# Performance work log

Hardware: AMD Instinct MI355X
Metric: run time of the kernel (lower is better)

## Reference

```python
import jax, jax.numpy as jnp
import numpy as np

RES = 192      # resolution
RANK = 8       # low-rank
FD = 32        # feature_dim
NFPD = 32      # num_features_per_dim = round(32768**(1/3))
RADIUS = 1.3
NI = 128       # n_intersections
STEP = 0.0352  # step_size
B = 2048       # rays


def setup_inputs():
    key = jax.random.key(0)
    ks = jax.random.split(key, 12)
    ro = jax.random.normal(ks[0], (B, 3), dtype=jnp.float32)
    ro = ro / jnp.linalg.norm(ro, axis=-1, keepdims=True) * 2.5  # origins outside the cube
    rd = -ro + 0.1 * jax.random.normal(ks[1], (B, 3), dtype=jnp.float32)
    rd = rd / jnp.linalg.norm(rd, axis=-1, keepdims=True)        # roughly toward origin
    def nrm(k, shape, std):
        return std * jax.random.normal(k, shape, dtype=jnp.float32)
    return {
        "rays_o": ro, "rays_d": rd,
        "Gxy": nrm(ks[2], (RES, RES, 3, RANK), 0.1),
        "Gxz": nrm(ks[3], (RES, RES, 3, RANK), 0.1),
        "Gyz": nrm(ks[4], (RES, RES, 3, RANK), 0.1),
        "F_grid": nrm(ks[5], (NFPD, NFPD, NFPD, FD), 0.05),
        "sW0": nrm(ks[6], (FD, 128), FD ** -0.5),
        "sW1": nrm(ks[7], (128, 128), 128 ** -0.5),
        "sW2": nrm(ks[8], (128, 16), 128 ** -0.5),
        "cW0": nrm(ks[9], (31, 64), 31 ** -0.5),
        "cW1": nrm(ks[10], (64, 64), 64 ** -0.5),
        "cW2": nrm(ks[11], (64, 3), 64 ** -0.5),
    }


def trilinear(vol, coords):
    # vol: [D,H,W,C]; coords: [N,3] as (x,y,z) in [-1,1]; x indexes W (last spatial dim)
    # matches torch grid_sample(align_corners=True, mode='bilinear', padding_mode='border')
    D, H, W, C = vol.shape
    def prep(c, size):
        idx = jnp.clip((c + 1.0) * 0.5 * (size - 1), 0.0, size - 1.0)  # border clamp
        i0 = jnp.clip(jnp.floor(idx).astype(jnp.int32), 0, size - 2)
        return i0, i0 + 1, idx - i0
    x0, x1, wx = prep(coords[:, 0], W)
    y0, y1, wy = prep(coords[:, 1], H)
    z0, z1, wz = prep(coords[:, 2], D)
    wx = wx[:, None]; wy = wy[:, None]; wz = wz[:, None]
    def g(zi, yi, xi):
        return vol[zi, yi, xi]  # [N,C]
    c00 = g(z0, y0, x0) * (1 - wx) + g(z0, y0, x1) * wx
    c01 = g(z0, y1, x0) * (1 - wx) + g(z0, y1, x1) * wx
    c10 = g(z1, y0, x0) * (1 - wx) + g(z1, y0, x1) * wx
    c11 = g(z1, y1, x0) * (1 - wx) + g(z1, y1, x1) * wx
    c0 = c00 * (1 - wy) + c01 * wy
    c1 = c10 * (1 - wy) + c11 * wy
    return c0 * (1 - wz) + c1 * wz


def sh16(d):
    # tcnn SphericalHarmonics degree 4 on directions (input (d+1)/2 is unmapped back to d internally)
    x, y, z = d[:, 0], d[:, 1], d[:, 2]
    x2, y2, z2 = x * x, y * y, z * z
    return jnp.stack([
        jnp.full_like(x, 0.28209479177387814),
        -0.48860251190291987 * y,
        0.48860251190291987 * z,
        -0.48860251190291987 * x,
        1.0925484305920792 * x * y,
        -1.0925484305920792 * y * z,
        0.94617469575755997 * z2 - 0.31539156525251999,
        -1.0925484305920792 * x * z,
        0.54627421529603959 * (x2 - y2),
        0.59004358992664352 * y * (-3.0 * x2 + y2),
        2.8906114426405538 * x * y * z,
        0.45704579946446572 * y * (1.0 - 5.0 * z2),
        0.3731763325901154 * z * (5.0 * z2 - 3.0),
        0.45704579946446572 * x * (1.0 - 5.0 * z2),
        1.445305721320277 * z * (x2 - y2),
        0.59004358992664352 * x * (-x2 + 3.0 * y2),
    ], axis=-1)


def _forward(rays_o, rays_d, Gxy, Gxz, Gyz, F_grid, sW0, sW1, sW2, cW0, cW1, cW2):
    b = rays_o.shape[0]
    # --- get_intersections: ray/AABB [-R,R]^3, uniform marching ---
    d = jnp.where(jnp.abs(rays_d) < 1e-9, 1e-9, rays_d)
    t1 = (-RADIUS - rays_o) / d
    t2 = (RADIUS - rays_o) / d
    tmin = jnp.max(jnp.minimum(t1, t2), axis=-1)
    tmax = jnp.min(jnp.maximum(t1, t2), axis=-1)
    near = jnp.maximum(tmin, 0.0)
    ts = near[:, None] + jnp.arange(NI + 1, dtype=jnp.float32) * STEP  # intersections [B,NI+1]
    tmid = 0.5 * (ts[:, :-1] + ts[:, 1:])                              # [B,NI]
    pts = rays_o[:, None, :] + tmid[..., None] * rays_d[:, None, :]    # [B,NI,3]
    mask = (jnp.all(jnp.abs(pts) <= RADIUS, axis=-1)
            & (tmid <= tmax[:, None]) & (tmax > tmin)[:, None])        # [B,NI]
    rdn = rays_d / jnp.linalg.norm(rays_d, axis=-1, keepdims=True)
    # coordinate chain of forward + eval_pts nets out to pts/RADIUS in [-1,1]
    p = ((pts / RADIUS + 1.0) * RES / 2.0) * 2.0 / RES - 1.0
    pf = p.reshape(-1, 3)
    # --- densify low-rank tri-plane grid: sum_r Gxy*Gxz*Gyz -> [RES,RES,RES,3] ---
    grid = jnp.zeros((RES, RES, RES, 3), dtype=Gxy.dtype)
    for r in range(RANK):  # fixed small rank; avoids a [RES^3,3,RANK] intermediate
        grid = grid + (Gxy[:, :, None, :, r] * Gxz[:, None, :, :, r] * Gyz[None, :, :, :, r])
    # --- eval_pts: grid_sample -> hash-feature grid_sample -> MLPs ---
    Gvals = trilinear(grid, pf)            # [N,3]
    Fvals = trilinear(F_grid, Gvals)       # [N,FD]
    h = jax.nn.relu(Fvals @ sW0)
    h = jax.nn.relu(h @ sW1)
    out16 = h @ sW2                        # [N,16]
    sigma = out16[:, 0].reshape(b, NI)
    sigma = jax.nn.relu(jnp.where(mask, sigma, 0.0))
    rdn_pts = jnp.broadcast_to(rdn[:, None, :], (b, NI, 3)).reshape(-1, 3)
    ci = jnp.concatenate([sh16(rdn_pts), out16[:, 1:]], axis=-1)  # [N,31]
    c = jax.nn.relu(ci @ cW0)
    c = jax.nn.relu(c @ cW1)
    color = (c @ cW2).reshape(b, NI, 3)
    color = jnp.where(mask[..., None], color, 0.0)
    # --- sigma2alpha + shrgb2rgb (white background) ---
    dists = ts[:, 1:] - ts[:, :-1]         # |rdn| == 1
    alpha = 1.0 - jnp.exp(-sigma * dists)
    T = jnp.cumprod(1.0 - alpha + 1e-10, axis=-1)
    T = jnp.concatenate([jnp.ones_like(T[:, :1]), T[:, :-1]], axis=-1)  # exclusive
    w = alpha * T                          # abs_light [B,NI]
    rgb = jax.nn.sigmoid(color)
    acc = jnp.sum(w, axis=-1)
    return jnp.sum(w[..., None] * rgb, axis=1) + (1.0 - acc)[..., None]  # [B,3]


def reference(rays_o, rays_d, Gxy, Gxz, Gyz, F_grid, sW0, sW1, sW2, cW0, cW1, cW2):
    return _forward(rays_o, rays_d, Gxy, Gxz, Gyz, F_grid, sW0, sW1, sW2, cW0, cW1, cW2)
```

## Files before the change

kernel.cpp:

```cpp
#include <hip/hip_runtime.h>
#include <math.h>

#define RES 192
#define RANK 8
#define NI 128
#define LW 136

typedef __attribute__((ext_vector_type(8))) _Float16 h8;
typedef __attribute__((ext_vector_type(2))) _Float16 h2f;
typedef __attribute__((ext_vector_type(4))) float floatx4;

#define OFF_SW0 0
#define OFF_SW1 4096
#define OFF_SW2 20480
#define OFF_CW0 22528
#define OFF_CW1 24576
#define OFF_CW2 28672
#define PACK_TOTAL 29696

#define TRI_CELLS (RES*RES)
#define TRI_TOTAL (3*TRI_CELLS*24)
#define FG_TOTAL  (32*32*32*32)
#define PREP_TOTAL (PACK_TOTAL + TRI_TOTAL + FG_TOTAL)

__device__ __forceinline__ void prep_idx(float c, int size, int& i0, float& f){
    float idx = (c + 1.0f)*0.5f*(float)(size-1);
    idx = fminf(fmaxf(idx, 0.0f), (float)(size-1));
    int ii = (int)idx;
    if (ii > size-2) ii = size-2;
    i0 = ii;
    f = idx - (float)ii;
}

__device__ __forceinline__ float wred64(float v){
    #pragma unroll
    for (int o=32;o>0;o>>=1) v += __shfl_down(v, o, 64);
    return v;
}

__global__ void __launch_bounds__(256) prep_all(
    const float* __restrict__ sW0, const float* __restrict__ sW1,
    const float* __restrict__ sW2, const float* __restrict__ cW0,
    const float* __restrict__ cW1, const float* __restrict__ cW2,
    const float* __restrict__ Gxy, const float* __restrict__ Gxz,
    const float* __restrict__ Gyz, const float* __restrict__ F_grid,
    _Float16* __restrict__ Wp, _Float16* __restrict__ Gp, _Float16* __restrict__ Fg)
{
    int e = blockIdx.x*256 + threadIdx.x;
    if (e < PACK_TOTAL){
        const float* src; int K, N, ksteps, base;
        if      (e < OFF_SW1){ src=sW0; K=32;  N=128; ksteps=1; base=OFF_SW0; }
        else if (e < OFF_SW2){ src=sW1; K=128; N=128; ksteps=4; base=OFF_SW1; }
        else if (e < OFF_CW0){ src=sW2; K=128; N=16;  ksteps=4; base=OFF_SW2; }
        else if (e < OFF_CW1){ src=cW0; K=31;  N=64;  ksteps=1; base=OFF_CW0; }
        else if (e < OFF_CW2){ src=cW1; K=64;  N=64;  ksteps=2; base=OFF_CW1; }
        else                 { src=cW2; K=64;  N=3;   ksteps=2; base=OFF_CW2; }
        int i = e - base;
        int j = i & 7, lane = (i>>3)&63, t = i>>9;
        int ks = t % ksteps, nt = t / ksteps;
        int k = ks*32 + (lane>>4)*8 + j;
        int n = nt*16 + (lane&15);
        float v = (k < K && n < N) ? src[k*N + n] : 0.0f;
        Wp[e] = (_Float16)v;
        return;
    }
    int e2 = e - PACK_TOTAL;
    if (e2 < TRI_TOTAL){
        int p    = e2 / (TRI_CELLS*24);
        int rem  = e2 - p*(TRI_CELLS*24);
        int cell = rem / 24;
        int c    = rem - cell*24;
        const float* src = (p==0) ? Gxy : (p==1) ? Gxz : Gyz;
        Gp[((size_t)(p*TRI_CELLS + cell))*32 + c] = (_Float16)src[(size_t)cell*24 + c];
        return;
    }
    int e3 = e2 - TRI_TOTAL;
    Fg[e3] = (_Float16)F_grid[e3];
}

__launch_bounds__(256, 4)
__global__ void nerf_fused(
    const float* __restrict__ rays_o, const float* __restrict__ rays_d,
    const _Float16* __restrict__ Gp, const _Float16* __restrict__ Fg,
    const _Float16* __restrict__ Wp, float* __restrict__ out)
{
    __shared__ _Float16 buf[128*LW];
    __shared__ float sigmaArr[128];
    __shared__ float rgbArr[128*3];
    __shared__ float wtot[2];
    __shared__ float partial[8];

    const int tid  = threadIdx.x;
    const int lane = tid & 63;
    const int wv   = tid >> 6;
    const int ray  = blockIdx.x;

    const float ox = rays_o[ray*3+0], oy = rays_o[ray*3+1], oz = rays_o[ray*3+2];
    const float dx = rays_d[ray*3+0], dy = rays_d[ray*3+1], dz = rays_d[ray*3+2];

    float sdx = (fabsf(dx) < 1e-9f) ? 1e-9f : dx;
    float sdy = (fabsf(dy) < 1e-9f) ? 1e-9f : dy;
    float sdz = (fabsf(dz) < 1e-9f) ? 1e-9f : dz;
    float t1x = (-1.3f - ox)/sdx, t2x = (1.3f - ox)/sdx;
    float t1y = (-1.3f - oy)/sdy, t2y = (1.3f - oy)/sdy;
    float t1z = (-1.3f - oz)/sdz, t2z = (1.3f - oz)/sdz;
    float tmin = fmaxf(fminf(t1x,t2x), fmaxf(fminf(t1y,t2y), fminf(t1z,t2z)));
    float tmax = fminf(fmaxf(t1x,t2x), fminf(fmaxf(t1y,t2y), fmaxf(t1z,t2z)));
    float nearv = fmaxf(tmin, 0.0f);

    const int rowbase = wv*32;
    const int col  = lane & 15;
    const int quad = lane >> 4;
    const int ar0  = rowbase + col;
    const int ar1  = ar0 + 16;

    {
        int sid = rowbase + (lane & 31);
        float w_ts0 = nearv + (float)sid     * 0.0352f;
        float w_ts1 = nearv + (float)(sid+1) * 0.0352f;
        float w_tm  = 0.5f*(w_ts0+w_ts1);
        float wpx = ox + w_tm*dx, wpy = oy + w_tm*dy, wpz = oz + w_tm*dz;
        bool m = (fabsf(wpx)<=1.3f) && (fabsf(wpy)<=1.3f) && (fabsf(wpz)<=1.3f)
               && (w_tm<=tmax) && (tmax>tmin);
        if (__ballot(m) == 0ULL) goto composite;
    }

    {
        const int s = rowbase + (lane >> 1);
        const int h = lane & 1;

        float ts0 = nearv + (float)s     * 0.0352f;
        float ts1 = nearv + (float)(s+1) * 0.0352f;
        float tmid = 0.5f*(ts0+ts1);
        float px = ox + tmid*dx, py = oy + tmid*dy, pz = oz + tmid*dz;
        bool mask = (fabsf(px)<=1.3f) && (fabsf(py)<=1.3f) && (fabsf(pz)<=1.3f)
                  && (tmid<=tmax) && (tmax>tmin);

        h8 FVa = {0,0,0,0,0,0,0,0};
        h8 FVb = {0,0,0,0,0,0,0,0};

        if (mask){
            float p0 = (px/1.3f + 1.0f)*192.0f/2.0f*2.0f/192.0f - 1.0f;
            float p1 = (py/1.3f + 1.0f)*192.0f/2.0f*2.0f/192.0f - 1.0f;
            float p2 = (pz/1.3f + 1.0f)*192.0f/2.0f*2.0f/192.0f - 1.0f;

            int x0, y0, z0; float fx, fy, fz;
            prep_idx(p0, RES, x0, fx);
            prep_idx(p1, RES, y0, fy);
            prep_idx(p2, RES, z0, fz);

            const int zi = z0 + h;
            const float wzc = h ? fz : (1.0f - fz);

            h8 XY[2][3], XZ[2][3], YZ[2][2][3];
            {
                const h8* pxy0 = (const h8*)(Gp + ((size_t)(zi*RES + y0  ))*32);
                const h8* pxy1 = (const h8*)(Gp + ((size_t)(zi*RES + y0+1))*32);
                const h8* pxz0 = (const h8*)(Gp + ((size_t)(TRI_CELLS + zi*RES + x0  ))*32);
                const h8* pxz1 = (const h8*)(Gp + ((size_t)(TRI_CELLS + zi*RES + x0+1))*32);
                const h8* pyz00 = (const h8*)(Gp + ((size_t)(2*TRI_CELLS + (y0  )*RES + x0  ))*32);
                const h8* pyz01 = (const h8*)(Gp + ((size_t)(2*TRI_CELLS + (y0  )*RES + x0+1))*32);
                const h8* pyz10 = (const h8*)(Gp + ((size_t)(2*TRI_CELLS + (y0+1)*RES + x0  ))*32);
                const h8* pyz11 = (const h8*)(Gp + ((size_t)(2*TRI_CELLS + (y0+1)*RES + x0+1))*32);
                #pragma unroll
                for (int q=0;q<3;q++){
                    XY[0][q]=pxy0[q]; XY[1][q]=pxy1[q];
                    XZ[0][q]=pxz0[q]; XZ[1][q]=pxz1[q];
                    YZ[0][0][q]=pyz00[q]; YZ[0][1][q]=pyz01[q];
                    YZ[1][0][q]=pyz10[q]; YZ[1][1][q]=pyz11[q];
                }
            }

            h8 ACC0 = {0,0,0,0,0,0,0,0};
            h8 ACC1 = {0,0,0,0,0,0,0,0};
            h8 ACC2 = {0,0,0,0,0,0,0,0};
            #pragma unroll
            for (int yc=0; yc<2; yc++){
                const float wy = yc ? fy : (1.0f - fy);
                #pragma unroll
                for (int xc=0; xc<2; xc++){
                    const float wx = xc ? fx : (1.0f - fx);
                    const _Float16 wh = (_Float16)(wzc*wy*wx);
                    const h8 w8 = {wh,wh,wh,wh,wh,wh,wh,wh};
                    h8 Q0 = (XY[yc][0]*XZ[xc][0])*YZ[yc][xc][0];
                    h8 Q1 = (XY[yc][1]*XZ[xc][1])*YZ[yc][xc][1];
                    h8 Q2 = (XY[yc][2]*XZ[xc][2])*YZ[yc][xc][2];
                    ACC0 = __builtin_elementwise_fma(Q0, w8, ACC0);
                    ACC1 = __builtin_elementwise_fma(Q1, w8, ACC1);
                    ACC2 = __builtin_elementwise_fma(Q2, w8, ACC2);
                }
            }
            h2f a0h = __builtin_shufflevector(ACC0,ACC0,0,1) + __builtin_shufflevector(ACC0,ACC0,2,3);
            h2f b0h = __builtin_shufflevector(ACC0,ACC0,4,5) + __builtin_shufflevector(ACC0,ACC0,6,7);
            h2f c0h = a0h + b0h;
            float gv0 = (float)c0h[0] + (float)c0h[1];
            h2f a1h = __builtin_shufflevector(ACC1,ACC1,0,1) + __builtin_shufflevector(ACC1,ACC1,2,3);
            h2f b1h = __builtin_shufflevector(ACC1,ACC1,4,5) + __builtin_shufflevector(ACC1,ACC1,6,7);
            h2f c1h = a1h + b1h;
            float gv1 = (float)c1h[0] + (float)c1h[1];
            h2f a2h = __builtin_shufflevector(ACC2,ACC2,0,1) + __builtin_shufflevector(ACC2,ACC2,2,3);
            h2f b2h = __builtin_shufflevector(ACC2,ACC2,4,5) + __builtin_shufflevector(ACC2,ACC2,6,7);
            h2f c2h = a2h + b2h;
            float gv2 = (float)c2h[0] + (float)c2h[1];

            gv0 += __shfl_xor(gv0, 1, 64);
            gv1 += __shfl_xor(gv1, 1, 64);
            gv2 += __shfl_xor(gv2, 1, 64);

            int a0,b0,c0; float fa,fb,fc;
            prep_idx(gv2, 32, a0, fa);
            prep_idx(gv1, 32, b0, fb);
            prep_idx(gv0, 32, c0, fc);
            #pragma unroll
            for (int zc=0; zc<2; zc++){
                const int zi2 = a0+zc; const float wz2 = zc ? fa : 1.f-fa;
                #pragma unroll
                for (int yc=0; yc<2; yc++){
                    const int yi2 = b0+yc; const float wy2 = yc ? fb : 1.f-fb;
                    #pragma unroll
                    for (int xc=0; xc<2; xc++){
                        const int xi2 = c0+xc; const float wx2 = xc ? fc : 1.f-fc;
                        const _Float16 wh = (_Float16)(wz2*wy2*wx2);
                        const h8 w8 = {wh,wh,wh,wh,wh,wh,wh,wh};
                        const h8* pf = (const h8*)(Fg + ((size_t)((zi2*32+yi2)*32+xi2))*32 + h*16);
                        FVa = __builtin_elementwise_fma(pf[0], w8, FVa);
                        FVb = __builtin_elementwise_fma(pf[1], w8, FVb);
                    }
                }
            }
        }

        *(h8*)&buf[s*LW + h*16]     = FVa;
        *(h8*)&buf[s*LW + h*16 + 8] = FVb;
    }

    {
        h8 a0 = *(const h8*)&buf[ar0*LW + quad*8];
        h8 a1 = *(const h8*)&buf[ar1*LW + quad*8];
        const h8* W = (const h8*)(Wp + OFF_SW0);
        #pragma unroll
        for (int nt=0; nt<8; nt++){
            h8 b = W[nt*64 + lane];
            floatx4 c0v = {0.f,0.f,0.f,0.f}, c1v = {0.f,0.f,0.f,0.f};
            c0v = __builtin_amdgcn_mfma_f32_16x16x32_f16(a0, b, c0v, 0,0,0);
            c1v = __builtin_amdgcn_mfma_f32_16x16x32_f16(a1, b, c1v, 0,0,0);
            #pragma unroll
            for (int r=0;r<4;r++){
                int row0 = rowbase + quad*4 + r;
                buf[row0*LW      + nt*16 + col] = (_Float16)fmaxf(c0v[r],0.f);
                buf[(row0+16)*LW + nt*16 + col] = (_Float16)fmaxf(c1v[r],0.f);
            }
        }
    }

    {
        h8 A0[4], A1[4];
        #pragma unroll
        for (int ks=0;ks<4;ks++){
            A0[ks] = *(const h8*)&buf[ar0*LW + ks*32 + quad*8];
            A1[ks] = *(const h8*)&buf[ar1*LW + ks*32 + quad*8];
        }
        const h8* W = (const h8*)(Wp + OFF_SW1);
        #pragma unroll
        for (int nt=0; nt<8; nt++){
            floatx4 c0v = {0.f,0.f,0.f,0.f}, c1v = {0.f,0.f,0.f,0.f};
            #pragma unroll
            for (int ks=0;ks<4;ks++){
                h8 b = W[(nt*4+ks)*64 + lane];
                c0v = __builtin_amdgcn_mfma_f32_16x16x32_f16(A0[ks], b, c0v, 0,0,0);
                c1v = __builtin_amdgcn_mfma_f32_16x16x32_f16(A1[ks], b, c1v, 0,0,0);
            }
            #pragma unroll
            for (int r=0;r<4;r++){
                int row0 = rowbase + quad*4 + r;
                buf[row0*LW      + nt*16 + col] = (_Float16)fmaxf(c0v[r],0.f);
                buf[(row0+16)*LW + nt*16 + col] = (_Float16)fmaxf(c1v[r],0.f);
            }
        }
    }

    {
        h8 A0[4], A1[4];
        #pragma unroll
        for (int ks=0;ks<4;ks++){
            A0[ks] = *(const h8*)&buf[ar0*LW + ks*32 + quad*8];
            A1[ks] = *(const h8*)&buf[ar1*LW + ks*32 + quad*8];
        }
        const h8* W = (const h8*)(Wp + OFF_SW2);
        floatx4 c0v = {0.f,0.f,0.f,0.f}, c1v = {0.f,0.f,0.f,0.f};
        #pragma unroll
        for (int ks=0;ks<4;ks++){
            h8 b = W[ks*64 + lane];
            c0v = __builtin_amdgcn_mfma_f32_16x16x32_f16(A0[ks], b, c0v, 0,0,0);
            c1v = __builtin_amdgcn_mfma_f32_16x16x32_f16(A1[ks], b, c1v, 0,0,0);
        }
        #pragma unroll
        for (int r=0;r<4;r++){
            int row0 = rowbase + quad*4 + r;
            if (col == 0){
                sigmaArr[row0]    = c0v[r];
                sigmaArr[row0+16] = c1v[r];
            } else {
                buf[row0*LW      + 15 + col] = (_Float16)c0v[r];
                buf[(row0+16)*LW + 15 + col] = (_Float16)c1v[r];
            }
        }
        const float dn = sqrtf(dx*dx+dy*dy+dz*dz);
        const float X = dx/dn, Y = dy/dn, Z = dz/dn;
        const float X2=X*X, Y2=Y*Y, Z2=Z*Z;
        float sh[16];
        sh[0]= 0.28209479177387814f;
        sh[1]=-0.48860251190291987f*Y;
        sh[2]= 0.48860251190291987f*Z;
        sh[3]=-0.48860251190291987f*X;
        sh[4]= 1.0925484305920792f*X*Y;
        sh[5]=-1.0925484305920792f*Y*Z;
        sh[6]= 0.94617469575756f*Z2 - 0.31539156525252f;
        sh[7]=-1.0925484305920792f*X*Z;
        sh[8]= 0.5462742152960396f*(X2-Y2);
        sh[9]= 0.5900435899266435f*Y*(-3.0f*X2+Y2);
        sh[10]=2.890611442640554f*X*Y*Z;
        sh[11]=0.4570457994644657f*Y*(1.0f-5.0f*Z2);
        sh[12]=0.3731763325901154f*Z*(5.0f*Z2-3.0f);
        sh[13]=0.4570457994644657f*X*(1.0f-5.0f*Z2);
        sh[14]=1.445305721320277f*Z*(X2-Y2);
        sh[15]=0.5900435899266435f*X*(-X2+3.0f*Y2);
        if (lane < 32){
            int row = rowbase + lane;
            #pragma unroll
            for (int k=0;k<16;k++) buf[row*LW + k] = (_Float16)sh[k];
        }
    }

    {
        h8 a0 = *(const h8*)&buf[ar0*LW + quad*8];
        h8 a1 = *(const h8*)&buf[ar1*LW + quad*8];
        const h8* W = (const h8*)(Wp + OFF_CW0);
        #pragma unroll
        for (int nt=0; nt<4; nt++){
            h8 b = W[nt*64 + lane];
            floatx4 c0v = {0.f,0.f,0.f,0.f}, c1v = {0.f,0.f,0.f,0.f};
            c0v = __builtin_amdgcn_mfma_f32_16x16x32_f16(a0, b, c0v, 0,0,0);
            c1v = __builtin_amdgcn_mfma_f32_16x16x32_f16(a1, b, c1v, 0,0,0);
            #pragma unroll
            for (int r=0;r<4;r++){
                int row0 = rowbase + quad*4 + r;
                buf[row0*LW      + nt*16 + col] = (_Float16)fmaxf(c0v[r],0.f);
                buf[(row0+16)*LW + nt*16 + col] = (_Float16)fmaxf(c1v[r],0.f);
            }
        }
    }

    {
        h8 A0[2], A1[2];
        #pragma unroll
        for (int ks=0;ks<2;ks++){
            A0[ks] = *(const h8*)&buf[ar0*LW + ks*32 + quad*8];
            A1[ks] = *(const h8*)&buf[ar1*LW + ks*32 + quad*8];
        }
        const h8* W = (const h8*)(Wp + OFF_CW1);
        #pragma unroll
        for (int nt=0; nt<4; nt++){
            floatx4 c0v = {0.f,0.f,0.f,0.f}, c1v = {0.f,0.f,0.f,0.f};
            #pragma unroll
            for (int ks=0;ks<2;ks++){
                h8 b = W[(nt*2+ks)*64 + lane];
                c0v = __builtin_amdgcn_mfma_f32_16x16x32_f16(A0[ks], b, c0v, 0,0,0);
                c1v = __builtin_amdgcn_mfma_f32_16x16x32_f16(A1[ks], b, c1v, 0,0,0);
            }
            #pragma unroll
            for (int r=0;r<4;r++){
                int row0 = rowbase + quad*4 + r;
                buf[row0*LW      + nt*16 + col] = (_Float16)fmaxf(c0v[r],0.f);
                buf[(row0+16)*LW + nt*16 + col] = (_Float16)fmaxf(c1v[r],0.f);
            }
        }
    }

    {
        h8 A0[2], A1[2];
        #pragma unroll
        for (int ks=0;ks<2;ks++){
            A0[ks] = *(const h8*)&buf[ar0*LW + ks*32 + quad*8];
            A1[ks] = *(const h8*)&buf[ar1*LW + ks*32 + quad*8];
        }
        const h8* W = (const h8*)(Wp + OFF_CW2);
        floatx4 c0v = {0.f,0.f,0.f,0.f}, c1v = {0.f,0.f,0.f,0.f};
        #pragma unroll
        for (int ks=0;ks<2;ks++){
            h8 b = W[ks*64 + lane];
            c0v = __builtin_amdgcn_mfma_f32_16x16x32_f16(A0[ks], b, c0v, 0,0,0);
            c1v = __builtin_amdgcn_mfma_f32_16x16x32_f16(A1[ks], b, c1v, 0,0,0);
        }
        if (col < 3){
            #pragma unroll
            for (int r=0;r<4;r++){
                int row0 = rowbase + quad*4 + r;
                rgbArr[row0*3 + col]      = c0v[r];
                rgbArr[(row0+16)*3 + col] = c1v[r];
            }
        }
    }

composite:
    __syncthreads();

    {
        float alpha = 0.f, rr = 0.f, rg = 0.f, rb = 0.f;
        if (tid < 128){
            float ts0 = nearv + (float)tid     * 0.0352f;
            float ts1 = nearv + (float)(tid+1) * 0.0352f;
            float tmid = 0.5f*(ts0+ts1);
            float dist = ts1 - ts0;
            float px = ox + tmid*dx, py = oy + tmid*dy, pz = oz + tmid*dz;
            bool mask = (fabsf(px)<=1.3f) && (fabsf(py)<=1.3f) && (fabsf(pz)<=1.3f)
                      && (tmid<=tmax) && (tmax>tmin);
            float sg = mask ? fmaxf(sigmaArr[tid], 0.f) : 0.f;
            alpha = 1.0f - expf(-sg*dist);
            if (mask){
                rr = 1.0f/(1.0f+expf(-rgbArr[tid*3+0]));
                rg = 1.0f/(1.0f+expf(-rgbArr[tid*3+1]));
                rb = 1.0f/(1.0f+expf(-rgbArr[tid*3+2]));
            }
        }
        float p = 1.0f - alpha + 1e-10f;
        #pragma unroll
        for (int off=1; off<64; off<<=1){
            float u = __shfl_up(p, off, 64);
            if (lane >= off) p *= u;
        }
        if (tid < 128 && lane == 63) wtot[wv] = p;
        float excl = __shfl_up(p, 1, 64);
        if (lane == 0) excl = 1.0f;
        __syncthreads();
        if (tid < 128){
            float T = excl;
            if (wv == 1) T *= wtot[0];
            float w = alpha * T;
            float v0 = wred64(w*rr);
            float v1 = wred64(w*rg);
            float v2 = wred64(w*rb);
            float v3 = wred64(w);
            if (lane == 0){
                partial[wv*4+0]=v0; partial[wv*4+1]=v1; partial[wv*4+2]=v2; partial[wv*4+3]=v3;
            }
        }
        __syncthreads();
        if (tid == 0){
            float acc = partial[3] + partial[7];
            float bg  = 1.0f - acc;
            out[ray*3+0] = partial[0] + partial[4] + bg;
            out[ray*3+1] = partial[1] + partial[5] + bg;
            out[ray*3+2] = partial[2] + partial[6] + bg;
        }
    }
}

extern "C" void kernel_launch(void* const* d_in, const int* in_sizes, int n_in,
                              void* d_out, int out_size, void* d_ws, size_t ws_size,
                              hipStream_t stream){
    const float* rays_o = (const float*)d_in[0];
    const float* rays_d = (const float*)d_in[1];
    const float* Gxy    = (const float*)d_in[2];
    const float* Gxz    = (const float*)d_in[3];
    const float* Gyz    = (const float*)d_in[4];
    const float* F_grid = (const float*)d_in[5];
    const float* sW0    = (const float*)d_in[6];
    const float* sW1    = (const float*)d_in[7];
    const float* sW2    = (const float*)d_in[8];
    const float* cW0    = (const float*)d_in[9];
    const float* cW1    = (const float*)d_in[10];
    const float* cW2    = (const float*)d_in[11];

    _Float16* Wp = (_Float16*)d_ws;
    _Float16* Gp = Wp + PACK_TOTAL;
    _Float16* Fg = Gp + (size_t)3*TRI_CELLS*32;

    prep_all<<<PREP_TOTAL/256, 256, 0, stream>>>(sW0,sW1,sW2,cW0,cW1,cW2,
                                                 Gxy,Gxz,Gyz,F_grid, Wp,Gp,Fg);
    nerf_fused<<<2048, 256, 0, stream>>>(rays_o, rays_d, Gp, Fg, Wp, (float*)d_out);
}
```

Measured before the change: 131.5 us.

## Split each ray's samples across eight waves with four lanes per sample

Doubles the block to 512 threads so each wave handles 16 samples instead of 32. Four lanes now cooperate on each sample: they split the (z,y) corners of the tri-plane gather and combine results with xor shuffles, and each takes an 8-channel slice of the feature-grid trilinear gather. The MLP stages then issue one MFMA row-tile per wave instead of two. The aim is more wavefronts to hide gather latency and fewer registers per thread. The cost is more shuffle reductions, possibly lower occupancy per CU because of the larger block and LDS use, and idle upper waves during compositing.

Result: slower. 138.8 us (+5.6%).

```diff
diff --git a/kernel.cpp b/kernel.cpp
--- a/kernel.cpp
+++ b/kernel.cpp
@@ -36,6 +36,13 @@
     #pragma unroll
     for (int o=32;o>0;o>>=1) v += __shfl_down(v, o, 64);
     return v;
+}
+
+__device__ __forceinline__ float hsum8(h8 a){
+    h2f x = __builtin_shufflevector(a,a,0,1) + __builtin_shufflevector(a,a,2,3);
+    h2f y = __builtin_shufflevector(a,a,4,5) + __builtin_shufflevector(a,a,6,7);
+    h2f z = x + y;
+    return (float)z[0] + (float)z[1];
 }
 
 __global__ void __launch_bounds__(256) prep_all(
@@ -78,7 +85,7 @@
     Fg[e3] = (_Float16)F_grid[e3];
 }
 
-__launch_bounds__(256, 4)
+__launch_bounds__(512, 8)
 __global__ void nerf_fused(
     const float* __restrict__ rays_o, const float* __restrict__ rays_d,
     const _Float16* __restrict__ Gp, const _Float16* __restrict__ Fg,
@@ -95,6 +102,11 @@
     const int wv   = tid >> 6;
     const int ray  = blockIdx.x;
 
+    const int rowbase = wv*16;
+    const int col  = lane & 15;
+    const int quad = lane >> 4;
+    const int ar   = rowbase + col;
+
     const float ox = rays_o[ray*3+0], oy = rays_o[ray*3+1], oz = rays_o[ray*3+2];
     const float dx = rays_d[ray*3+0], dy = rays_d[ray*3+1], dz = rays_d[ray*3+2];
 
@@ -108,316 +120,248 @@
     float tmax = fminf(fmaxf(t1x,t2x), fminf(fmaxf(t1y,t2y), fmaxf(t1z,t2z)));
     float nearv = fmaxf(tmin, 0.0f);
 
-    const int rowbase = wv*32;
-    const int col  = lane & 15;
-    const int quad = lane >> 4;
-    const int ar0  = rowbase + col;
-    const int ar1  = ar0 + 16;
-
-    {
-        int sid = rowbase + (lane & 31);
-        float w_ts0 = nearv + (float)sid     * 0.0352f;
-        float w_ts1 = nearv + (float)(sid+1) * 0.0352f;
-        float w_tm  = 0.5f*(w_ts0+w_ts1);
-        float wpx = ox + w_tm*dx, wpy = oy + w_tm*dy, wpz = oz + w_tm*dz;
-        bool m = (fabsf(wpx)<=1.3f) && (fabsf(wpy)<=1.3f) && (fabsf(wpz)<=1.3f)
-               && (w_tm<=tmax) && (tmax>tmin);
-        if (__ballot(m) == 0ULL) goto composite;
+    const int s   = rowbase + (lane >> 2);
+    const int sub = lane & 3;
+    const int zc  = sub & 1;
+    const int yc  = sub >> 1;
+
+    float ts0 = nearv + (float)s     * 0.0352f;
+    float ts1 = nearv + (float)(s+1) * 0.0352f;
+    float tmid = 0.5f*(ts0+ts1);
+    float px = ox + tmid*dx, py = oy + tmid*dy, pz = oz + tmid*dz;
+    bool mask = (fabsf(px)<=1.3f) && (fabsf(py)<=1.3f) && (fabsf(pz)<=1.3f)
+              && (tmid<=tmax) && (tmax>tmin);
+
+    if (__ballot(mask) != 0ULL){
+        {
+            h8 FV = {0,0,0,0,0,0,0,0};
+            if (mask){
+                float p0 = (px/1.3f + 1.0f)*192.0f/2.0f*2.0f/192.0f - 1.0f;
+                float p1 = (py/1.3f + 1.0f)*192.0f/2.0f*2.0f/192.0f - 1.0f;
+                float p2 = (pz/1.3f + 1.0f)*192.0f/2.0f*2.0f/192.0f - 1.0f;
+
+                int x0, y0, z0; float fx, fy, fz;
+                prep_idx(p0, RES, x0, fx);
+                prep_idx(p1, RES, y0, fy);
+                prep_idx(p2, RES, z0, fz);
+
+                const int zi = z0 + zc;
+                const int yi = y0 + yc;
+                const float wzy = (zc ? fz : 1.0f-fz) * (yc ? fy : 1.0f-fy);
+
+                h8 XYc[3], XZ0[3], XZ1[3], YZ0[3], YZ1[3];
+                {
+                    const h8* pxy = (const h8*)(Gp + ((size_t)(zi*RES + yi))*32);
+                    const h8* px0 = (const h8*)(Gp + ((size_t)(TRI_CELLS + zi*RES + x0  ))*32);
+                    const h8* px1 = (const h8*)(Gp + ((size_t)(TRI_CELLS + zi*RES + x0+1))*32);
+                    const h8* py0 = (const h8*)(Gp + ((size_t)(2*TRI_CELLS + yi*RES + x0  ))*32);
+                    const h8* py1 = (const h8*)(Gp + ((size_t)(2*TRI_CELLS + yi*RES + x0+1))*32);
+                    #pragma unroll
+                    for (int q=0;q<3;q++){
+                        XYc[q]=pxy[q];
+                        XZ0[q]=px0[q]; XZ1[q]=px1[q];
+                        YZ0[q]=py0[q]; YZ1[q]=py1[q];
+                    }
+                }
+
+                h8 ACC0, ACC1, ACC2;
+                {
+                    const _Float16 w0 = (_Float16)(wzy*(1.0f-fx));
+                    const _Float16 w1 = (_Float16)(wzy*fx);
+                    const h8 w80 = {w0,w0,w0,w0,w0,w0,w0,w0};
+                    const h8 w81 = {w1,w1,w1,w1,w1,w1,w1,w1};
+                    ACC0 = (XYc[0]*XZ0[0])*YZ0[0]*w80;
+                    ACC1 = (XYc[1]*XZ0[1])*YZ0[1]*w80;
+                    ACC2 = (XYc[2]*XZ0[2])*YZ0[2]*w80;
+                    ACC0 = __builtin_elementwise_fma((XYc[0]*XZ1[0])*YZ1[0], w81, ACC0);
+                    ACC1 = __builtin_elementwise_fma((XYc[1]*XZ1[1])*YZ1[1], w81, ACC1);
+                    ACC2 = __builtin_elementwise_fma((XYc[2]*XZ1[2])*YZ1[2], w81, ACC2);
+                }
+                float gv0 = hsum8(ACC0);
+                float gv1 = hsum8(ACC1);
+                float gv2 = hsum8(ACC2);
+                gv0 += __shfl_xor(gv0, 1, 64); gv0 += __shfl_xor(gv0, 2, 64);
+                gv1 += __shfl_xor(gv1, 1, 64); gv1 += __shfl_xor(gv1, 2, 64);
+                gv2 += __shfl_xor(gv2, 1, 64); gv2 += __shfl_xor(gv2, 2, 64);
+
+                int a0,b0,c0; float fa,fb,fc;
+                prep_idx(gv2, 32, a0, fa);
+                prep_idx(gv1, 32, b0, fb);
+                prep_idx(gv0, 32, c0, fc);
+                #pragma unroll
+                for (int zc2=0; zc2<2; zc2++){
+                    const int zi2 = a0+zc2; const float wz2 = zc2 ? fa : 1.f-fa;
+                    #pragma unroll
+                    for (int yc2=0; yc2<2; yc2++){
+                        const int yi2 = b0+yc2; const float wy2 = yc2 ? fb : 1.f-fb;
+                        #pragma unroll
+                        for (int xc2=0; xc2<2; xc2++){
+                            const int xi2 = c0+xc2; const float wx2 = xc2 ? fc : 1.f-fc;
+                            const _Float16 wh = (_Float16)(wz2*wy2*wx2);
+                            const h8 w8 = {wh,wh,wh,wh,wh,wh,wh,wh};
+                            const h8* pf = (const h8*)(Fg + ((size_t)((zi2*32+yi2)*32+xi2))*32 + sub*8);
+                            FV = __builtin_elementwise_fma(pf[0], w8, FV);
+                        }
+                    }
+                }
+            }
+            *(h8*)&buf[s*LW + sub*8] = FV;
+        }
+
+        {
+            h8 a = *(const h8*)&buf[ar*LW + quad*8];
+            const h8* W = (const h8*)(Wp + OFF_SW0);
+            #pragma unroll
+            for (int nt=0; nt<8; nt++){
+                h8 b = W[nt*64 + lane];
+                floatx4 cv = {0.f,0.f,0.f,0.f};
+                cv = __builtin_amdgcn_mfma_f32_16x16x32_f16(a, b, cv, 0,0,0);
+                #pragma unroll
+                for (int r=0;r<4;r++){
+                    int row = rowbase + quad*4 + r;
+                    buf[row*LW + nt*16 + col] = (_Float16)fmaxf(cv[r],0.f);
+                }
+            }
+        }
+
+        {
+            h8 A[4];
+            #pragma unroll
+            for (int ks=0;ks<4;ks++) A[ks] = *(const h8*)&buf[ar*LW + ks*32 + quad*8];
+            const h8* W = (const h8*)(Wp + OFF_SW1);
+            #pragma unroll
+            for (int nt=0; nt<8; nt++){
+                floatx4 cv = {0.f,0.f,0.f,0.f};
+                #pragma unroll
+                for (int ks=0;ks<4;ks++){
+                    h8 b = W[(nt*4+ks)*64 + lane];
+                    cv = __builtin_amdgcn_mfma_f32_16x16x32_f16(A[ks], b, cv, 0,0,0);
+                }
+                #pragma unroll
+                for (int r=0;r<4;r++){
+                    int row = rowbase + quad*4 + r;
+                    buf[row*LW + nt*16 + col] = (_Float16)fmaxf(cv[r],0.f);
+                }
+            }
+        }
+
+        {
+            h8 A[4];
+            #pragma unroll
+            for (int ks=0;ks<4;ks++) A[ks] = *(const h8*)&buf[ar*LW + ks*32 + quad*8];
+            const h8* W = (const h8*)(Wp + OFF_SW2);
+            floatx4 cv = {0.f,0.f,0.f,0.f};
+            #pragma unroll
+            for (int ks=0;ks<4;ks++){
+                h8 b = W[ks*64 + lane];
+                cv = __builtin_amdgcn_mfma_f32_16x16x32_f16(A[ks], b, cv, 0,0,0);
+            }
+            #pragma unroll
+            for (int r=0;r<4;r++){
+                int row = rowbase + quad*4 + r;
+                if (col == 0) sigmaArr[row] = cv[r];
+                else          buf[row*LW + 15 + col] = (_Float16)cv[r];
+            }
+            const float dn = sqrtf(dx*dx+dy*dy+dz*dz);
+            const float X = dx/dn, Y = dy/dn, Z = dz/dn;
+            const float X2=X*X, Y2=Y*Y, Z2=Z*Z;
+            float sh[16];
+            sh[0]= 0.28209479177387814f;
+            sh[1]=-0.48860251190291987f*Y;
+            sh[2]= 0.48860251190291987f*Z;
+            sh[3]=-0.48860251190291987f*X;
+            sh[4]= 1.0925484305920792f*X*Y;
+            sh[5]=-1.0925484305920792f*Y*Z;
+            sh[6]= 0.94617469575756f*Z2 - 0.31539156525252f;
+            sh[7]=-1.0925484305920792f*X*Z;
+            sh[8]= 0.5462742152960396f*(X2-Y2);
+            sh[9]= 0.5900435899266435f*Y*(-3.0f*X2+Y2);
+            sh[10]=2.890611442640554f*X*Y*Z;
+            sh[11]=0.4570457994644657f*Y*(1.0f-5.0f*Z2);
+            sh[12]=0.3731763325901154f*Z*(5.0f*Z2-3.0f);
+            sh[13]=0.4570457994644657f*X*(1.0f-5.0f*Z2);
+            sh[14]=1.445305721320277f*Z*(X2-Y2);
+            sh[15]=0.5900435899266435f*X*(-X2+3.0f*Y2);
+            if (lane < 16){
+                int row = rowbase + lane;
+                #pragma unroll
+                for (int k=0;k<16;k++) buf[row*LW + k] = (_Float16)sh[k];
+            }
+        }
+
+        {
+            h8 a = *(const h8*)&buf[ar*LW + quad*8];
+            const h8* W = (const h8*)(Wp + OFF_CW0);
+            #pragma unroll
+            for (int nt=0; nt<4; nt++){
+                h8 b = W[nt*64 + lane];
+                floatx4 cv = {0.f,0.f,0.f,0.f};
+                cv = __builtin_amdgcn_mfma_f32_16x16x32_f16(a, b, cv, 0,0,0);
+                #pragma unroll
+                for (int r=0;r<4;r++){
+                    int row = rowbase + quad*4 + r;
+                    buf[row*LW + nt*16 + col] = (_Float16)fmaxf(cv[r],0.f);
+                }
+            }
+        }
+
+        {
+            h8 A[2];
+            #pragma unroll
+            for (int ks=0;ks<2;ks++) A[ks] = *(const h8*)&buf[ar*LW + ks*32 + quad*8];
+            const h8* W = (const h8*)(Wp + OFF_CW1);
+            #pragma unroll
+            for (int nt=0; nt<4; nt++){
+                floatx4 cv = {0.f,0.f,0.f,0.f};
+                #pragma unroll
+                for (int ks=0;ks<2;ks++){
+                    h8 b = W[(nt*2+ks)*64 + lane];
+                    cv = __builtin_amdgcn_mfma_f32_16x16x32_f16(A[ks], b, cv, 0,0,0);
+                }
+                #pragma unroll
+                for (int r=0;r<4;r++){
+                    int row = rowbase + quad*4 + r;
+                    buf[row*LW + nt*16 + col] = (_Float16)fmaxf(cv[r],0.f);
+                }
+            }
+        }
+
+        {
+            h8 A[2];
+            #pragma unroll
+            for (int ks=0;ks<2;ks++) A[ks] = *(const h8*)&buf[ar*LW + ks*32 + quad*8];
+            const h8* W = (const h8*)(Wp + OFF_CW2);
+            floatx4 cv = {0.f,0.f,0.f,0.f};
+            #pragma unroll
+            for (int ks=0;ks<2;ks++){
+                h8 b = W[ks*64 + lane];
+                cv = __builtin_amdgcn_mfma_f32_16x16x32_f16(A[ks], b, cv, 0,0,0);
+            }
+            if (col < 3){
+                #pragma unroll
+                for (int r=0;r<4;r++){
+                    int row = rowbase + quad*4 + r;
+                    rgbArr[row*3 + col] = cv[r];
+                }
+            }
+        }
     }
 
-    {
-        const int s = rowbase + (lane >> 1);
-        const int h = lane & 1;
-
-        float ts0 = nearv + (float)s     * 0.0352f;
-        float ts1 = nearv + (float)(s+1) * 0.0352f;
-        float tmid = 0.5f*(ts0+ts1);
-        float px = ox + tmid*dx, py = oy + tmid*dy, pz = oz + tmid*dz;
-        bool mask = (fabsf(px)<=1.3f) && (fabsf(py)<=1.3f) && (fabsf(pz)<=1.3f)
-                  && (tmid<=tmax) && (tmax>tmin);
-
-        h8 FVa = {0,0,0,0,0,0,0,0};
-        h8 FVb = {0,0,0,0,0,0,0,0};
-
-        if (mask){
-            float p0 = (px/1.3f + 1.0f)*192.0f/2.0f*2.0f/192.0f - 1.0f;
-            float p1 = (py/1.3f + 1.0f)*192.0f/2.0f*2.0f/192.0f - 1.0f;
-            float p2 = (pz/1.3f + 1.0f)*192.0f/2.0f*2.0f/192.0f - 1.0f;
-
-            int x0, y0, z0; float fx, fy, fz;
-            prep_idx(p0, RES, x0, fx);
-            prep_idx(p1, RES, y0, fy);
-            prep_idx(p2, RES, z0, fz);
-
-            const int zi = z0 + h;
-            const float wzc = h ? fz : (1.0f - fz);
-
-            h8 XY[2][3], XZ[2][3], YZ[2][2][3];
-            {
-                const h8* pxy0 = (const h8*)(Gp + ((size_t)(zi*RES + y0  ))*32);
-                const h8* pxy1 = (const h8*)(Gp + ((size_t)(zi*RES + y0+1))*32);
-                const h8* pxz0 = (const h8*)(Gp + ((size_t)(TRI_CELLS + zi*RES + x0  ))*32);
-                const h8* pxz1 = (const h8*)(Gp + ((size_t)(TRI_CELLS + zi*RES + x0+1))*32);
-                const h8* pyz00 = (const h8*)(Gp + ((size_t)(2*TRI_CELLS + (y0  )*RES + x0  ))*32);
-                const h8* pyz01 = (const h8*)(Gp + ((size_t)(2*TRI_CELLS + (y0  )*RES + x0+1))*32);
-                const h8* pyz10 = (const h8*)(Gp + ((size_t)(2*TRI_CELLS + (y0+1)*RES + x0  ))*32);
-                const h8* pyz11 = (const h8*)(Gp + ((size_t)(2*TRI_CELLS + (y0+1)*RES + x0+1))*32);
-                #pragma unroll
-                for (int q=0;q<3;q++){
-                    XY[0][q]=pxy0[q]; XY[1][q]=pxy1[q];
-                    XZ[0][q]=pxz0[q]; XZ[1][q]=pxz1[q];
-                    YZ[0][0][q]=pyz00[q]; YZ[0][1][q]=pyz01[q];
-                    YZ[1][0][q]=pyz10[q]; YZ[1][1][q]=pyz11[q];
-                }
-            }
-
-            h8 ACC0 = {0,0,0,0,0,0,0,0};
-            h8 ACC1 = {0,0,0,0,0,0,0,0};
-            h8 ACC2 = {0,0,0,0,0,0,0,0};
-            #pragma unroll
-            for (int yc=0; yc<2; yc++){
-                const float wy = yc ? fy : (1.0f - fy);
-                #pragma unroll
-                for (int xc=0; xc<2; xc++){
-                    const float wx = xc ? fx : (1.0f - fx);
-                    const _Float16 wh = (_Float16)(wzc*wy*wx);
-                    const h8 w8 = {wh,wh,wh,wh,wh,wh,wh,wh};
-                    h8 Q0 = (XY[yc][0]*XZ[xc][0])*YZ[yc][xc][0];
-                    h8 Q1 = (XY[yc][1]*XZ[xc][1])*YZ[yc][xc][1];
-                    h8 Q2 = (XY[yc][2]*XZ[xc][2])*YZ[yc][xc][2];
-                    ACC0 = __builtin_elementwise_fma(Q0, w8, ACC0);
-                    ACC1 = __builtin_elementwise_fma(Q1, w8, ACC1);
-                    ACC2 = __builtin_elementwise_fma(Q2, w8, ACC2);
-                }
-            }
-            h2f a0h = __builtin_shufflevector(ACC0,ACC0,0,1) + __builtin_shufflevector(ACC0,ACC0,2,3);
-            h2f b0h = __builtin_shufflevector(ACC0,ACC0,4,5) + __builtin_shufflevector(ACC0,ACC0,6,7);
-            h2f c0h = a0h + b0h;
-            float gv0 = (float)c0h[0] + (float)c0h[1];
-            h2f a1h = __builtin_shufflevector(ACC1,ACC1,0,1) + __builtin_shufflevector(ACC1,ACC1,2,3);
-            h2f b1h = __builtin_shufflevector(ACC1,ACC1,4,5) + __builtin_shufflevector(ACC1,ACC1,6,7);
-            h2f c1h = a1h + b1h;
-            float gv1 = (float)c1h[0] + (float)c1h[1];
-            h2f a2h = __builtin_shufflevector(ACC2,ACC2,0,1) + __builtin_shufflevector(ACC2,ACC2,2,3);
-            h2f b2h = __builtin_shufflevector(ACC2,ACC2,4,5) + __builtin_shufflevector(ACC2,ACC2,6,7);
-            h2f c2h = a2h + b2h;
-            float gv2 = (float)c2h[0] + (float)c2h[1];
-
-            gv0 += __shfl_xor(gv0, 1, 64);
-            gv1 += __shfl_xor(gv1, 1, 64);
-            gv2 += __shfl_xor(gv2, 1, 64);
-
-            int a0,b0,c0; float fa,fb,fc;
-            prep_idx(gv2, 32, a0, fa);
-            prep_idx(gv1, 32, b0, fb);
-            prep_idx(gv0, 32, c0, fc);
-            #pragma unroll
-            for (int zc=0; zc<2; zc++){
-                const int zi2 = a0+zc; const float wz2 = zc ? fa : 1.f-fa;
-                #pragma unroll
-                for (int yc=0; yc<2; yc++){
-                    const int yi2 = b0+yc; const float wy2 = yc ? fb : 1.f-fb;
-                    #pragma unroll
-                    for (int xc=0; xc<2; xc++){
-                        const int xi2 = c0+xc; const float wx2 = xc ? fc : 1.f-fc;
-                        const _Float16 wh = (_Float16)(wz2*wy2*wx2);
-                        const h8 w8 = {wh,wh,wh,wh,wh,wh,wh,wh};
-                        const h8* pf = (const h8*)(Fg + ((size_t)((zi2*32+yi2)*32+xi2))*32 + h*16);
-                        FVa = __builtin_elementwise_fma(pf[0], w8, FVa);
-                        FVb = __builtin_elementwise_fma(pf[1], w8, FVb);
-                    }
-                }
-            }
-        }
-
-        *(h8*)&buf[s*LW + h*16]     = FVa;
-        *(h8*)&buf[s*LW + h*16 + 8] = FVb;
-    }
-
-    {
-        h8 a0 = *(const h8*)&buf[ar0*LW + quad*8];
-        h8 a1 = *(const h8*)&buf[ar1*LW + quad*8];
-        const h8* W = (const h8*)(Wp + OFF_SW0);
-        #pragma unroll
-        for (int nt=0; nt<8; nt++){
-            h8 b = W[nt*64 + lane];
-            floatx4 c0v = {0.f,0.f,0.f,0.f}, c1v = {0.f,0.f,0.f,0.f};
-            c0v = __builtin_amdgcn_mfma_f32_16x16x32_f16(a0, b, c0v, 0,0,0);
-            c1v = __builtin_amdgcn_mfma_f32_16x16x32_f16(a1, b, c1v, 0,0,0);
-            #pragma unroll
-            for (int r=0;r<4;r++){
-                int row0 = rowbase + quad*4 + r;
-                buf[row0*LW      + nt*16 + col] = (_Float16)fmaxf(c0v[r],0.f);
-                buf[(row0+16)*LW + nt*16 + col] = (_Float16)fmaxf(c1v[r],0.f);
-            }
-        }
-    }
-
-    {
-        h8 A0[4], A1[4];
-        #pragma unroll
-        for (int ks=0;ks<4;ks++){
-            A0[ks] = *(const h8*)&buf[ar0*LW + ks*32 + quad*8];
-            A1[ks] = *(const h8*)&buf[ar1*LW + ks*32 + quad*8];
-        }
-        const h8* W = (const h8*)(Wp + OFF_SW1);
-        #pragma unroll
-        for (int nt=0; nt<8; nt++){
-            floatx4 c0v = {0.f,0.f,0.f,0.f}, c1v = {0.f,0.f,0.f,0.f};
-            #pragma unroll
-            for (int ks=0;ks<4;ks++){
-                h8 b = W[(nt*4+ks)*64 + lane];
-                c0v = __builtin_amdgcn_mfma_f32_16x16x32_f16(A0[ks], b, c0v, 0,0,0);
-                c1v = __builtin_amdgcn_mfma_f32_16x16x32_f16(A1[ks], b, c1v, 0,0,0);
-            }
-            #pragma unroll
-            for (int r=0;r<4;r++){
-                int row0 = rowbase + quad*4 + r;
-                buf[row0*LW      + nt*16 + col] = (_Float16)fmaxf(c0v[r],0.f);
-                buf[(row0+16)*LW + nt*16 + col] = (_Float16)fmaxf(c1v[r],0.f);
-            }
-        }
-    }
-
-    {
-        h8 A0[4], A1[4];
-        #pragma unroll
-        for (int ks=0;ks<4;ks++){
-            A0[ks] = *(const h8*)&buf[ar0*LW + ks*32 + quad*8];
-            A1[ks] = *(const h8*)&buf[ar1*LW + ks*32 + quad*8];
-        }
-        const h8* W = (const h8*)(Wp + OFF_SW2);
-        floatx4 c0v = {0.f,0.f,0.f,0.f}, c1v = {0.f,0.f,0.f,0.f};
-        #pragma unroll
-        for (int ks=0;ks<4;ks++){
-            h8 b = W[ks*64 + lane];
-            c0v = __builtin_amdgcn_mfma_f32_16x16x32_f16(A0[ks], b, c0v, 0,0,0);
-            c1v = __builtin_amdgcn_mfma_f32_16x16x32_f16(A1[ks], b, c1v, 0,0,0);
-        }
-        #pragma unroll
-        for (int r=0;r<4;r++){
-            int row0 = rowbase + quad*4 + r;
-            if (col == 0){
-                sigmaArr[row0]    = c0v[r];
-                sigmaArr[row0+16] = c1v[r];
-            } else {
-                buf[row0*LW      + 15 + col] = (_Float16)c0v[r];
-                buf[(row0+16)*LW + 15 + col] = (_Float16)c1v[r];
-            }
-        }
-        const float dn = sqrtf(dx*dx+dy*dy+dz*dz);
-        const float X = dx/dn, Y = dy/dn, Z = dz/dn;
-        const float X2=X*X, Y2=Y*Y, Z2=Z*Z;
-        float sh[16];
-        sh[0]= 0.28209479177387814f;
-        sh[1]=-0.48860251190291987f*Y;
-        sh[2]= 0.48860251190291987f*Z;
-        sh[3]=-0.48860251190291987f*X;
-        sh[4]= 1.0925484305920792f*X*Y;
-        sh[5]=-1.0925484305920792f*Y*Z;
-        sh[6]= 0.94617469575756f*Z2 - 0.31539156525252f;
-        sh[7]=-1.0925484305920792f*X*Z;
-        sh[8]= 0.5462742152960396f*(X2-Y2);
-        sh[9]= 0.5900435899266435f*Y*(-3.0f*X2+Y2);
-        sh[10]=2.890611442640554f*X*Y*Z;
-        sh[11]=0.4570457994644657f*Y*(1.0f-5.0f*Z2);
-        sh[12]=0.3731763325901154f*Z*(5.0f*Z2-3.0f);
-        sh[13]=0.4570457994644657f*X*(1.0f-5.0f*Z2);
-        sh[14]=1.445305721320277f*Z*(X2-Y2);
-        sh[15]=0.5900435899266435f*X*(-X2+3.0f*Y2);
-        if (lane < 32){
-            int row = rowbase + lane;
-            #pragma unroll
-            for (int k=0;k<16;k++) buf[row*LW + k] = (_Float16)sh[k];
-        }
-    }
-
-    {
-        h8 a0 = *(const h8*)&buf[ar0*LW + quad*8];
-        h8 a1 = *(const h8*)&buf[ar1*LW + quad*8];
-        const h8* W = (const h8*)(Wp + OFF_CW0);
-        #pragma unroll
-        for (int nt=0; nt<4; nt++){
-            h8 b = W[nt*64 + lane];
-            floatx4 c0v = {0.f,0.f,0.f,0.f}, c1v = {0.f,0.f,0.f,0.f};
-            c0v = __builtin_amdgcn_mfma_f32_16x16x32_f16(a0, b, c0v, 0,0,0);
-            c1v = __builtin_amdgcn_mfma_f32_16x16x32_f16(a1, b, c1v, 0,0,0);
-            #pragma unroll
-            for (int r=0;r<4;r++){
-                int row0 = rowbase + quad*4 + r;
-                buf[row0*LW      + nt*16 + col] = (_Float16)fmaxf(c0v[r],0.f);
-                buf[(row0+16)*LW + nt*16 + col] = (_Float16)fmaxf(c1v[r],0.f);
-            }
-        }
-    }
-
-    {
-        h8 A0[2], A1[2];
-        #pragma unroll
-        for (int ks=0;ks<2;ks++){
-            A0[ks] = *(const h8*)&buf[ar0*LW + ks*32 + quad*8];
-            A1[ks] = *(const h8*)&buf[ar1*LW + ks*32 + quad*8];
-        }
-        const h8* W = (const h8*)(Wp + OFF_CW1);
-        #pragma unroll
-        for (int nt=0; nt<4; nt++){
-            floatx4 c0v = {0.f,0.f,0.f,0.f}, c1v = {0.f,0.f,0.f,0.f};
-            #pragma unroll
-            for (int ks=0;ks<2;ks++){
-                h8 b = W[(nt*2+ks)*64 + lane];
-                c0v = __builtin_amdgcn_mfma_f32_16x16x32_f16(A0[ks], b, c0v, 0,0,0);
-                c1v = __builtin_amdgcn_mfma_f32_16x16x32_f16(A1[ks], b, c1v, 0,0,0);
-            }
-            #pragma unroll
-            for (int r=0;r<4;r++){
-                int row0 = rowbase + quad*4 + r;
-                buf[row0*LW      + nt*16 + col] = (_Float16)fmaxf(c0v[r],0.f);
-                buf[(row0+16)*LW + nt*16 + col] = (_Float16)fmaxf(c1v[r],0.f);
-            }
-        }
-    }
-
-    {
-        h8 A0[2], A1[2];
-        #pragma unroll
-        for (int ks=0;ks<2;ks++){
-            A0[ks] = *(const h8*)&buf[ar0*LW + ks*32 + quad*8];
-            A1[ks] = *(const h8*)&buf[ar1*LW + ks*32 + quad*8];
-        }
-        const h8* W = (const h8*)(Wp + OFF_CW2);
-        floatx4 c0v = {0.f,0.f,0.f,0.f}, c1v = {0.f,0.f,0.f,0.f};
-        #pragma unroll
-        for (int ks=0;ks<2;ks++){
-            h8 b = W[ks*64 + lane];
-            c0v = __builtin_amdgcn_mfma_f32_16x16x32_f16(A0[ks], b, c0v, 0,0,0);
-            c1v = __builtin_amdgcn_mfma_f32_16x16x32_f16(A1[ks], b, c1v, 0,0,0);
-        }
-        if (col < 3){
-            #pragma unroll
-            for (int r=0;r<4;r++){
-                int row0 = rowbase + quad*4 + r;
-                rgbArr[row0*3 + col]      = c0v[r];
-                rgbArr[(row0+16)*3 + col] = c1v[r];
-            }
-        }
-    }
-
-composite:
     __syncthreads();
 
     {
         float alpha = 0.f, rr = 0.f, rg = 0.f, rb = 0.f;
         if (tid < 128){
-            float ts0 = nearv + (float)tid     * 0.0352f;
-            float ts1 = nearv + (float)(tid+1) * 0.0352f;
-            float tmid = 0.5f*(ts0+ts1);
-            float dist = ts1 - ts0;
-            float px = ox + tmid*dx, py = oy + tmid*dy, pz = oz + tmid*dz;
-            bool mask = (fabsf(px)<=1.3f) && (fabsf(py)<=1.3f) && (fabsf(pz)<=1.3f)
-                      && (tmid<=tmax) && (tmax>tmin);
-            float sg = mask ? fmaxf(sigmaArr[tid], 0.f) : 0.f;
+            float cts0 = nearv + (float)tid     * 0.0352f;
+            float cts1 = nearv + (float)(tid+1) * 0.0352f;
+            float ctm  = 0.5f*(cts0+cts1);
+            float dist = cts1 - cts0;
+            float cpx = ox + ctm*dx, cpy = oy + ctm*dy, cpz = oz + ctm*dz;
+            bool cmask = (fabsf(cpx)<=1.3f) && (fabsf(cpy)<=1.3f) && (fabsf(cpz)<=1.3f)
+                       && (ctm<=tmax) && (tmax>tmin);
+            float sg = cmask ? fmaxf(sigmaArr[tid], 0.f) : 0.f;
             alpha = 1.0f - expf(-sg*dist);
-            if (mask){
+            if (cmask){
                 rr = 1.0f/(1.0f+expf(-rgbArr[tid*3+0]));
                 rg = 1.0f/(1.0f+expf(-rgbArr[tid*3+1]));
                 rb = 1.0f/(1.0f+expf(-rgbArr[tid*3+2]));
@@ -478,5 +422,5 @@
 
     prep_all<<<PREP_TOTAL/256, 256, 0, stream>>>(sW0,sW1,sW2,cW0,cW1,cW2,
                                                  Gxy,Gxz,Gyz,F_grid, Wp,Gp,Fg);
-    nerf_fused<<<2048, 256, 0, stream>>>(rays_o, rays_d, Gp, Fg, Wp, (float*)d_out);
-}
+    nerf_fused<<<2048, 512, 0, stream>>>(rays_o, rays_d, Gp, Fg, Wp, (float*)d_out);
+}
```
